# Kernel tuning notes

Hardware: AMD Instinct MI355X
Metric: run time of the kernel (lower is better)

## Reference

```python
import jax, jax.numpy as jnp
import numpy as np

B, C, T = 128, 9, 2048
R = T // 4            # reduced_timesteps after two MaxPool1d(2)
N = B * R             # total graph nodes
E_SINGLE = 8192       # edges per sample graph (avg degree 16 over R nodes)
HID = 128
OUT = 12


def setup_inputs():
    key = jax.random.key(0)
    ks = jax.random.split(key, 14)
    x = jax.random.normal(ks[0], (B, C, T), jnp.float32)
    # per-sample graph, replicated with offset i*R per batch element (as in forward)
    single = jax.random.randint(ks[1], (2, E_SINGLE), 0, R)
    offsets = (jnp.arange(B) * R)[None, :, None]
    edge_index = (single[:, None, :] + offsets).reshape(2, -1)  # [2, B*E_SINGLE]

    def lin(k, fan_in, shape):
        return jax.random.normal(k, shape, jnp.float32) / np.sqrt(fan_in)

    return {
        "x": x,
        "edge_index": edge_index,
        "conv1_w": lin(ks[2], C * 5, (16, C, 5)),
        "conv1_b": jnp.zeros((16,), jnp.float32),
        "conv2_w": lin(ks[3], 16 * 5, (32, 16, 5)),
        "conv2_b": jnp.zeros((32,), jnp.float32),
        "gcn1_w": lin(ks[4], 32, (32, HID)),
        "gcn1_b": jnp.zeros((HID,), jnp.float32),
        "gcn2_w": lin(ks[5], HID, (HID, HID)),
        "gcn2_b": jnp.zeros((HID,), jnp.float32),
        "fc_w": lin(ks[6], HID, (HID, OUT)),
        "fc_b": jnp.zeros((OUT,), jnp.float32),
    }


def _gcn_conv(h, edge_index, w, b, n):
    # PyG GCNConv: linear -> add self-loops -> sym-normalized sum aggregation -> + bias
    h = h @ w
    loops = jnp.arange(n)
    row = jnp.concatenate([edge_index[0], loops])  # source
    col = jnp.concatenate([edge_index[1], loops])  # target (aggregation)
    deg = jax.ops.segment_sum(jnp.ones(col.shape, h.dtype), col, num_segments=n)
    dis = jnp.where(deg > 0, jax.lax.rsqrt(jnp.maximum(deg, 1e-12)), 0.0)
    norm = dis[row] * dis[col]                      # [E+N]
    out = jax.ops.segment_sum(norm[:, None] * h[row], col, num_segments=n)
    return out + b


def _temporal_conv(x, w1, b1, w2, b2):
    dn = ("NCH", "OIH", "NCH")
    h = jax.lax.conv_general_dilated(x, w1, (1,), [(2, 2)], dimension_numbers=dn)
    h = jax.nn.relu(h + b1[None, :, None])
    h = jax.lax.reduce_window(h, -jnp.inf, jax.lax.max, (1, 1, 2), (1, 1, 2), "VALID")
    h = jax.lax.conv_general_dilated(h, w2, (1,), [(2, 2)], dimension_numbers=dn)
    h = jax.nn.relu(h + b2[None, :, None])
    h = jax.lax.reduce_window(h, -jnp.inf, jax.lax.max, (1, 1, 2), (1, 1, 2), "VALID")
    return h  # [B, 32, R]


def reference(x, edge_index, conv1_w, conv1_b, conv2_w, conv2_b,
              gcn1_w, gcn1_b, gcn2_w, gcn2_b, fc_w, fc_b):
    h = _temporal_conv(x, conv1_w, conv1_b, conv2_w, conv2_b)   # [B, 32, R]
    nodes = h.transpose(0, 2, 1).reshape(B * R, 32)             # [N, 32]
    g = jax.nn.relu(_gcn_conv(nodes, edge_index, gcn1_w, gcn1_b, N))
    g = jax.nn.relu(_gcn_conv(g, edge_index, gcn2_w, gcn2_b, N))
    g = g.reshape(B, R, HID).mean(axis=1)                       # [B, HID]
    return g @ fc_w + fc_b                                      # [B, OUT]
```

## Files before the change

kernel.cpp:

```cpp
#include <hip/hip_runtime.h>
#include <hip/hip_bf16.h>

#define BB   128
#define CIN  9
#define TT   2048
#define RR   512
#define NN   (BB*RR)
#define HID  128
#define NOUT 12

__global__ __launch_bounds__(256) void k_convs(const float* __restrict__ x,
        const float* __restrict__ w1, const float* __restrict__ b1,
        const float* __restrict__ w2, const float* __restrict__ b2,
        float* __restrict__ nodes, int* __restrict__ cnt,
        float* __restrict__ meanbuf) {
    __shared__ float sx[CIN][524];
    __shared__ float s1[16][260];
    __shared__ float sw1[16 * CIN * 5];
    __shared__ float sb1[16];
    __shared__ float sw2[32 * 16 * 5];
    __shared__ float sb2[32];
    int b  = blockIdx.x >> 2;
    int r0 = (blockIdx.x & 3) * 128;
    int tid = threadIdx.x;

    if (blockIdx.x == 0) { cnt[tid] = 0; cnt[tid + 256] = 0; }
    if (blockIdx.x < 64) meanbuf[blockIdx.x * 256 + tid] = 0.f;

    for (int idx = tid; idx < CIN * 524; idx += 256) {
        int c = idx / 524, j = idx - c * 524;
        int g = 4 * r0 - 6 + j;
        float v = 0.f;
        if (g >= 0 && g < TT) v = x[(b * CIN + c) * TT + g];
        sx[c][j] = v;
    }
    for (int idx = tid; idx < 16 * CIN * 5; idx += 256) sw1[idx] = w1[idx];
    for (int idx = tid; idx < 32 * 16 * 5; idx += 256) sw2[idx] = w2[idx];
    if (tid < 16) sb1[tid] = b1[tid];
    if (tid < 32) sb2[tid] = b2[tid];
    __syncthreads();

    for (int idx = tid; idx < 16 * 260; idx += 256) {
        int c1 = idx / 260, pp = idx - c1 * 260;
        int p = 2 * r0 - 2 + pp;
        float val = 0.f;
        if (p >= 0 && p < 1024) {
            float a0 = sb1[c1], a1 = a0;
#pragma unroll
            for (int c = 0; c < CIN; ++c) {
                float xv[6];
#pragma unroll
                for (int k = 0; k < 6; ++k) xv[k] = sx[c][2 * pp + k];
#pragma unroll
                for (int k = 0; k < 5; ++k) {
                    float wv = sw1[(c1 * CIN + c) * 5 + k];
                    a0 += xv[k]     * wv;
                    a1 += xv[k + 1] * wv;
                }
            }
            val = fmaxf(fmaxf(a0, a1), 0.f);
        }
        s1[c1][pp] = val;
    }
    __syncthreads();

    int rl   = tid & 127;
    int half = tid >> 7;
    float acc0[16], acc1[16];
#pragma unroll
    for (int o = 0; o < 16; ++o) { float bv = sb2[half * 16 + o]; acc0[o] = bv; acc1[o] = bv; }
#pragma unroll
    for (int c = 0; c < 16; ++c) {
        float xv[6];
#pragma unroll
        for (int k = 0; k < 6; ++k) xv[k] = s1[c][2 * rl + k];
#pragma unroll
        for (int o = 0; o < 16; ++o) {
            int oo = half * 16 + o;
#pragma unroll
            for (int k = 0; k < 5; ++k) {
                float wv = sw2[(oo * 16 + c) * 5 + k];
                acc0[o] += xv[k]     * wv;
                acc1[o] += xv[k + 1] * wv;
            }
        }
    }
    int n = b * RR + r0 + rl;
#pragma unroll
    for (int o = 0; o < 16; ++o) {
        int oo = half * 16 + o;
        nodes[n * 32 + oo] = fmaxf(fmaxf(acc0[o], acc1[o]), 0.f);
    }
}

__global__ __launch_bounds__(256) void k_deg512(const int* __restrict__ ei, int E,
        int es, int* __restrict__ cnt) {
    int i = blockIdx.x * 256 + threadIdx.x;
    if (i < es) atomicAdd(&cnt[ei[E + i]], 1);
}

__global__ __launch_bounds__(512) void k_scan512(const int* __restrict__ cnt, int es,
        int* __restrict__ rptr, int* __restrict__ cursor, float* __restrict__ dis) {
    __shared__ int sp[512];
    int t = threadIdx.x;
    int c = cnt[t];
    sp[t] = c;
    __syncthreads();
    for (int off = 1; off < 512; off <<= 1) {
        int v = sp[t];
        int add = (t >= off) ? sp[t - off] : 0;
        __syncthreads();
        sp[t] = v + add;
        __syncthreads();
    }
    int excl = sp[t] - c;
    rptr[t] = excl;
    cursor[t] = excl;
    if (t == 511) rptr[512] = es;
    dis[t] = rsqrtf((float)c + 1.0f);
}

__global__ __launch_bounds__(256) void k_scatter512(const int* __restrict__ ei, int E,
        int es, int* __restrict__ cursor, int* __restrict__ adj) {
    int i = blockIdx.x * 256 + threadIdx.x;
    if (i >= es) return;
    int row = ei[i];
    int col = ei[E + i];
    int pos = atomicAdd(&cursor[col], 1);
    adj[pos] = row;
}

__global__ __launch_bounds__(256) void k_gl1(const int* __restrict__ rptr,
        const int* __restrict__ adj, const float* __restrict__ dis,
        const float* __restrict__ nodes, const float* __restrict__ w,
        const float* __restrict__ bias, float* __restrict__ h) {
    __shared__ float srow[32][32];
    __shared__ float sw[32 * 128];
    int bid = (blockIdx.x & 7) * 256 + (blockIdx.x >> 3);
    int tid = threadIdx.x;
    int nbase = bid * 32;
    int b = nbase >> 9;
    const float* hb = nodes + (size_t)b * RR * 32;

    {
        const float4* src = (const float4*)w;
        float4* dst = (float4*)sw;
#pragma unroll
        for (int i = 0; i < 4; ++i) dst[tid + i * 256] = src[tid + i * 256];
    }

    int ln   = tid >> 3;
    int lane = tid & 7;
    int r = (nbase & 511) + ln;
    int s = rptr[r], e = rptr[r + 1];
    float dn = dis[r];
    float4 acc = make_float4(0.f, 0.f, 0.f, 0.f);
    for (int base = s; base < e; base += 8) {
        int j = base + lane;
        int src = 0; float nd = 0.f;
        if (j < e) { src = adj[j]; nd = dis[src]; }
        int cnt = min(8, e - base);
        int k = 0;
        for (; k + 4 <= cnt; k += 4) {
            int   s0 = __shfl(src, k, 8),     s1 = __shfl(src, k + 1, 8);
            int   s2 = __shfl(src, k + 2, 8), s3 = __shfl(src, k + 3, 8);
            float n0 = __shfl(nd, k, 8),      n1 = __shfl(nd, k + 1, 8);
            float n2 = __shfl(nd, k + 2, 8),  n3 = __shfl(nd, k + 3, 8);
            float4 v0 = *(const float4*)&hb[(size_t)s0 * 32 + lane * 4];
            float4 v1 = *(const float4*)&hb[(size_t)s1 * 32 + lane * 4];
            float4 v2 = *(const float4*)&hb[(size_t)s2 * 32 + lane * 4];
            float4 v3 = *(const float4*)&hb[(size_t)s3 * 32 + lane * 4];
            float w0 = dn * n0, w1 = dn * n1, w2 = dn * n2, w3 = dn * n3;
            acc.x += w0*v0.x + w1*v1.x + w2*v2.x + w3*v3.x;
            acc.y += w0*v0.y + w1*v1.y + w2*v2.y + w3*v3.y;
            acc.z += w0*v0.z + w1*v1.z + w2*v2.z + w3*v3.z;
            acc.w += w0*v0.w + w1*v1.w + w2*v2.w + w3*v3.w;
        }
        for (; k < cnt; ++k) {
            int   sk = __shfl(src, k, 8);
            float nk = __shfl(nd, k, 8);
            float4 v = *(const float4*)&hb[(size_t)sk * 32 + lane * 4];
            float wgt = dn * nk;
            acc.x += wgt * v.x; acc.y += wgt * v.y;
            acc.z += wgt * v.z; acc.w += wgt * v.w;
        }
    }
    {
        float4 v = *(const float4*)&hb[(size_t)r * 32 + lane * 4];
        float wgt = dn * dn;
        acc.x += wgt * v.x; acc.y += wgt * v.y;
        acc.z += wgt * v.z; acc.w += wgt * v.w;
    }
    *(float4*)&srow[ln][lane * 4] = acc;
    __syncthreads();

    int fq = tid & 31;
    int ng = tid >> 5;
    float a[4][4];
#pragma unroll
    for (int j = 0; j < 4; ++j)
#pragma unroll
        for (int q = 0; q < 4; ++q) a[j][q] = 0.f;
#pragma unroll
    for (int c = 0; c < 32; ++c) {
        float4 wv = *(const float4*)&sw[c * 128 + fq * 4];
#pragma unroll
        for (int j = 0; j < 4; ++j) {
            float xc = srow[ng * 4 + j][c];
            a[j][0] += xc * wv.x; a[j][1] += xc * wv.y;
            a[j][2] += xc * wv.z; a[j][3] += xc * wv.w;
        }
    }
    float4 bv = *(const float4*)&bias[fq * 4];
#pragma unroll
    for (int j = 0; j < 4; ++j) {
        float4 rr = make_float4(fmaxf(a[j][0] + bv.x, 0.f),
                                fmaxf(a[j][1] + bv.y, 0.f),
                                fmaxf(a[j][2] + bv.z, 0.f),
                                fmaxf(a[j][3] + bv.w, 0.f));
        *(float4*)&h[(size_t)(nbase + ng * 4 + j) * 128 + fq * 4] = rr;
    }
}

__global__ __launch_bounds__(256) void k_lin2(const float* __restrict__ g,
        const float* __restrict__ w, float* __restrict__ h) {
    __shared__ float srow[32 * 128];
    __shared__ float swc[64 * 128];
    int tid = threadIdx.x;
    int nbase = blockIdx.x * 32;
    {
        const float4* src = (const float4*)(g + (size_t)nbase * 128);
        float4* dst = (float4*)srow;
#pragma unroll
        for (int i = 0; i < 4; ++i) dst[tid + i * 256] = src[tid + i * 256];
    }
    int fq = tid & 31;
    int ng = tid >> 5;
    float acc[4][4];
#pragma unroll
    for (int j = 0; j < 4; ++j)
#pragma unroll
        for (int q = 0; q < 4; ++q) acc[j][q] = 0.f;

    for (int ch = 0; ch < 2; ++ch) {
        if (ch) __syncthreads();
        {
            const float4* src = (const float4*)(w + ch * 64 * 128);
            float4* dst = (float4*)swc;
#pragma unroll
            for (int i = 0; i < 8; ++i) dst[tid + i * 256] = src[tid + i * 256];
        }
        __syncthreads();
        int c0 = ch * 64;
#pragma unroll
        for (int c = 0; c < 64; ++c) {
            float4 wv = *(const float4*)&swc[c * 128 + fq * 4];
#pragma unroll
            for (int j = 0; j < 4; ++j) {
                float xc = srow[(ng * 4 + j) * 128 + c0 + c];
                acc[j][0] += xc * wv.x; acc[j][1] += xc * wv.y;
                acc[j][2] += xc * wv.z; acc[j][3] += xc * wv.w;
            }
        }
    }
#pragma unroll
    for (int j = 0; j < 4; ++j) {
        float4 r = make_float4(acc[j][0], acc[j][1], acc[j][2], acc[j][3]);
        *(float4*)&h[(size_t)(nbase + ng * 4 + j) * 128 + fq * 4] = r;
    }
}

__global__ __launch_bounds__(256) void k_gather128(const int* __restrict__ rptr,
        const int* __restrict__ adj, const float* __restrict__ dis,
        const float* __restrict__ h, const float* __restrict__ bias,
        float* __restrict__ meanbuf) {
    __shared__ float sred[8][128];
    int bid  = (blockIdx.x & 7) * 1024 + (blockIdx.x >> 3);
    int tid  = threadIdx.x;
    int g    = tid >> 5;
    int lane = tid & 31;
    int node = bid * 8 + g;
    int b = node >> 9;
    int r = node & 511;
    const float* hb = h + (size_t)b * RR * 128;
    int s = rptr[r], e = rptr[r + 1];
    float dn = dis[r];
    float4 acc = make_float4(0.f, 0.f, 0.f, 0.f);
    for (int base = s; base < e; base += 32) {
        int j = base + lane;
        int src = 0; float nd = 0.f;
        if (j < e) { src = adj[j]; nd = dis[src]; }
        int cnt = min(32, e - base);
        int k = 0;
        for (; k + 4 <= cnt; k += 4) {
            int   s0 = __shfl(src, k, 32),     s1 = __shfl(src, k + 1, 32);
            int   s2 = __shfl(src, k + 2, 32), s3 = __shfl(src, k + 3, 32);
            float n0 = __shfl(nd, k, 32),      n1 = __shfl(nd, k + 1, 32);
            float n2 = __shfl(nd, k + 2, 32),  n3 = __shfl(nd, k + 3, 32);
            float4 v0 = *(const float4*)&hb[(size_t)s0 * 128 + lane * 4];
            float4 v1 = *(const float4*)&hb[(size_t)s1 * 128 + lane * 4];
            float4 v2 = *(const float4*)&hb[(size_t)s2 * 128 + lane * 4];
            float4 v3 = *(const float4*)&hb[(size_t)s3 * 128 + lane * 4];
            float w0 = dn * n0, w1 = dn * n1, w2 = dn * n2, w3 = dn * n3;
            acc.x += w0*v0.x + w1*v1.x + w2*v2.x + w3*v3.x;
            acc.y += w0*v0.y + w1*v1.y + w2*v2.y + w3*v3.y;
            acc.z += w0*v0.z + w1*v1.z + w2*v2.z + w3*v3.z;
            acc.w += w0*v0.w + w1*v1.w + w2*v2.w + w3*v3.w;
        }
        for (; k < cnt; ++k) {
            int   sk = __shfl(src, k, 32);
            float nk = __shfl(nd, k, 32);
            float4 v = *(const float4*)&hb[(size_t)sk * 128 + lane * 4];
            float wgt = dn * nk;
            acc.x += wgt * v.x; acc.y += wgt * v.y;
            acc.z += wgt * v.z; acc.w += wgt * v.w;
        }
    }
    float4 v = *(const float4*)&hb[(size_t)r * 128 + lane * 4];
    float wgt = dn * dn;
    float4 bv = *(const float4*)&bias[lane * 4];
    acc.x = fmaxf(acc.x + wgt * v.x + bv.x, 0.f);
    acc.y = fmaxf(acc.y + wgt * v.y + bv.y, 0.f);
    acc.z = fmaxf(acc.z + wgt * v.z + bv.z, 0.f);
    acc.w = fmaxf(acc.w + wgt * v.w + bv.w, 0.f);
    *(float4*)&sred[g][lane * 4] = acc;
    __syncthreads();
    if (tid < 128) {
        float ssum = 0.f;
#pragma unroll
        for (int j = 0; j < 8; ++j) ssum += sred[j][tid];
        int sample = bid >> 6;
        unsafeAtomicAdd(&meanbuf[sample * 128 + tid], ssum * (1.0f / RR));
    }
}

__global__ __launch_bounds__(128) void k_fc(const float* __restrict__ meanbuf,
        const float* __restrict__ fw, const float* __restrict__ fb,
        float* __restrict__ out) {
    __shared__ float sm[HID];
    int b = blockIdx.x, f = threadIdx.x;
    sm[f] = meanbuf[b * HID + f];
    __syncthreads();
    if (f < NOUT) {
        float s = fb[f];
#pragma unroll
        for (int c = 0; c < HID; ++c) s += sm[c] * fw[c * NOUT + f];
        out[b * NOUT + f] = s;
    }
}

extern "C" void kernel_launch(void* const* d_in, const int* in_sizes, int n_in,
                              void* d_out, int out_size, void* d_ws, size_t ws_size,
                              hipStream_t stream) {
    const float* x   = (const float*)d_in[0];
    const int*   ei  = (const int*)d_in[1];
    const float* c1w = (const float*)d_in[2];
    const float* c1b = (const float*)d_in[3];
    const float* c2w = (const float*)d_in[4];
    const float* c2b = (const float*)d_in[5];
    const float* g1w = (const float*)d_in[6];
    const float* g1b = (const float*)d_in[7];
    const float* g2w = (const float*)d_in[8];
    const float* g2b = (const float*)d_in[9];
    const float* fw  = (const float*)d_in[10];
    const float* fb  = (const float*)d_in[11];
    float* out = (float*)d_out;
    int E  = in_sizes[1] / 2;
    int es = E / BB;

    char* ws = (char*)d_ws;
    float* nodes   = (float*)(ws);
    float* bufA    = (float*)(ws + (8u  << 20));
    float* bufC    = (float*)(ws + (40u << 20));
    int*   cnt     = (int*)  (ws + (72u << 20));
    int*   rptr    = (int*)  (ws + (72u << 20) + 4096);
    int*   cursor  = (int*)  (ws + (72u << 20) + 8192);
    float* dis     = (float*)(ws + (72u << 20) + 12288);
    int*   adj     = (int*)  (ws + (72u << 20) + 16384);
    float* meanbuf = (float*)(ws + (73u << 20));

    k_convs<<<BB * 4, 256, 0, stream>>>(x, c1w, c1b, c2w, c2b, nodes, cnt, meanbuf);

    k_deg512<<<(es + 255) / 256, 256, 0, stream>>>(ei, E, es, cnt);
    k_scan512<<<1, 512, 0, stream>>>(cnt, es, rptr, cursor, dis);
    k_scatter512<<<(es + 255) / 256, 256, 0, stream>>>(ei, E, es, cursor, adj);

    k_gl1<<<NN / 32, 256, 0, stream>>>(rptr, adj, dis, nodes, g1w, g1b, bufA);

    k_lin2<<<NN / 32, 256, 0, stream>>>(bufA, g2w, bufC);
    k_gather128<<<NN / 8, 256, 0, stream>>>(rptr, adj, dis, bufC, g2b, meanbuf);

    k_fc<<<BB, 128, 0, stream>>>(meanbuf, fw, fb, out);
}
```

Baseline: 212.4 us.

## Store GCN hidden activations in bf16, use MFMA for layer-2 linear, fuse CSR build

Hidden activations between the GCN layers are now stored as bf16, which halves the memory traffic of the layer-2 linear step and the neighbour gather. The second linear layer moves from scalar FP32 FMAs to bf16 MFMA 16x16x32 instructions, with the weight transposed into shared memory. The three CSR-build kernels (degree count, scan, scatter) are merged into a single one-block kernel that uses shared-memory atomics. Costs: reduced precision in the intermediates, each block re-converting the weights, and a serialised single-block graph build.

```diff
diff --git a/kernel.cpp b/kernel.cpp
--- a/kernel.cpp
+++ b/kernel.cpp
@@ -9,11 +9,22 @@
 #define HID  128
 #define NOUT 12
 
+typedef __attribute__((ext_vector_type(8))) short short8;
+typedef __attribute__((ext_vector_type(4))) float f32x4;
+
+static __device__ inline unsigned short f2bf(float f) {
+    unsigned int u = __float_as_uint(f);
+    unsigned int r = (u + 0x7fffu + ((u >> 16) & 1u)) >> 16;
+    return (unsigned short)r;
+}
+static __device__ inline float bf2f(unsigned short u) {
+    return __uint_as_float(((unsigned int)u) << 16);
+}
+
 __global__ __launch_bounds__(256) void k_convs(const float* __restrict__ x,
         const float* __restrict__ w1, const float* __restrict__ b1,
         const float* __restrict__ w2, const float* __restrict__ b2,
-        float* __restrict__ nodes, int* __restrict__ cnt,
-        float* __restrict__ meanbuf) {
+        float* __restrict__ nodes, float* __restrict__ meanbuf) {
     __shared__ float sx[CIN][524];
     __shared__ float s1[16][260];
     __shared__ float sw1[16 * CIN * 5];
@@ -24,7 +35,6 @@
     int r0 = (blockIdx.x & 3) * 128;
     int tid = threadIdx.x;
 
-    if (blockIdx.x == 0) { cnt[tid] = 0; cnt[tid + 256] = 0; }
     if (blockIdx.x < 64) meanbuf[blockIdx.x * 256 + tid] = 0.f;
 
     for (int idx = tid; idx < CIN * 524; idx += 256) {
@@ -93,17 +103,18 @@
     }
 }
 
-__global__ __launch_bounds__(256) void k_deg512(const int* __restrict__ ei, int E,
-        int es, int* __restrict__ cnt) {
-    int i = blockIdx.x * 256 + threadIdx.x;
-    if (i < es) atomicAdd(&cnt[ei[E + i]], 1);
-}
-
-__global__ __launch_bounds__(512) void k_scan512(const int* __restrict__ cnt, int es,
-        int* __restrict__ rptr, int* __restrict__ cursor, float* __restrict__ dis) {
+__global__ __launch_bounds__(512) void k_graph(const int* __restrict__ ei, int E,
+        int es, int* __restrict__ rptr, float* __restrict__ dis,
+        int* __restrict__ adj) {
+    __shared__ int lcnt[512];
     __shared__ int sp[512];
+    __shared__ int lcur[512];
     int t = threadIdx.x;
-    int c = cnt[t];
+    lcnt[t] = 0;
+    __syncthreads();
+    for (int i = t; i < es; i += 512) atomicAdd(&lcnt[ei[E + i]], 1);
+    __syncthreads();
+    int c = lcnt[t];
     sp[t] = c;
     __syncthreads();
     for (int off = 1; off < 512; off <<= 1) {
@@ -115,25 +126,21 @@
     }
     int excl = sp[t] - c;
     rptr[t] = excl;
-    cursor[t] = excl;
     if (t == 511) rptr[512] = es;
     dis[t] = rsqrtf((float)c + 1.0f);
-}
-
-__global__ __launch_bounds__(256) void k_scatter512(const int* __restrict__ ei, int E,
-        int es, int* __restrict__ cursor, int* __restrict__ adj) {
-    int i = blockIdx.x * 256 + threadIdx.x;
-    if (i >= es) return;
-    int row = ei[i];
-    int col = ei[E + i];
-    int pos = atomicAdd(&cursor[col], 1);
-    adj[pos] = row;
+    lcur[t] = excl;
+    __syncthreads();
+    for (int i = t; i < es; i += 512) {
+        int row = ei[i], col = ei[E + i];
+        int pos = atomicAdd(&lcur[col], 1);
+        adj[pos] = row;
+    }
 }
 
 __global__ __launch_bounds__(256) void k_gl1(const int* __restrict__ rptr,
         const int* __restrict__ adj, const float* __restrict__ dis,
         const float* __restrict__ nodes, const float* __restrict__ w,
-        const float* __restrict__ bias, float* __restrict__ h) {
+        const float* __restrict__ bias, unsigned short* __restrict__ h16) {
     __shared__ float srow[32][32];
     __shared__ float sw[32 * 128];
     int bid = (blockIdx.x & 7) * 256 + (blockIdx.x >> 3);
@@ -214,65 +221,73 @@
     float4 bv = *(const float4*)&bias[fq * 4];
 #pragma unroll
     for (int j = 0; j < 4; ++j) {
-        float4 rr = make_float4(fmaxf(a[j][0] + bv.x, 0.f),
-                                fmaxf(a[j][1] + bv.y, 0.f),
-                                fmaxf(a[j][2] + bv.z, 0.f),
-                                fmaxf(a[j][3] + bv.w, 0.f));
-        *(float4*)&h[(size_t)(nbase + ng * 4 + j) * 128 + fq * 4] = rr;
-    }
-}
-
-__global__ __launch_bounds__(256) void k_lin2(const float* __restrict__ g,
-        const float* __restrict__ w, float* __restrict__ h) {
-    __shared__ float srow[32 * 128];
-    __shared__ float swc[64 * 128];
+        ushort4 o;
+        o.x = f2bf(fmaxf(a[j][0] + bv.x, 0.f));
+        o.y = f2bf(fmaxf(a[j][1] + bv.y, 0.f));
+        o.z = f2bf(fmaxf(a[j][2] + bv.z, 0.f));
+        o.w = f2bf(fmaxf(a[j][3] + bv.w, 0.f));
+        *(ushort4*)&h16[(size_t)(nbase + ng * 4 + j) * 128 + fq * 4] = o;
+    }
+}
+
+__global__ __launch_bounds__(256) void k_lin2(const unsigned short* __restrict__ g16,
+        const float* __restrict__ w, unsigned short* __restrict__ h16) {
+    __shared__ unsigned short srow[64][136];
+    __shared__ unsigned short swT[128][136];
     int tid = threadIdx.x;
-    int nbase = blockIdx.x * 32;
+    int nbase = blockIdx.x * 64;
+
     {
-        const float4* src = (const float4*)(g + (size_t)nbase * 128);
-        float4* dst = (float4*)srow;
-#pragma unroll
-        for (int i = 0; i < 4; ++i) dst[tid + i * 256] = src[tid + i * 256];
-    }
-    int fq = tid & 31;
-    int ng = tid >> 5;
-    float acc[4][4];
-#pragma unroll
-    for (int j = 0; j < 4; ++j)
-#pragma unroll
-        for (int q = 0; q < 4; ++q) acc[j][q] = 0.f;
-
-    for (int ch = 0; ch < 2; ++ch) {
-        if (ch) __syncthreads();
-        {
-            const float4* src = (const float4*)(w + ch * 64 * 128);
-            float4* dst = (float4*)swc;
-#pragma unroll
-            for (int i = 0; i < 8; ++i) dst[tid + i * 256] = src[tid + i * 256];
-        }
-        __syncthreads();
-        int c0 = ch * 64;
-#pragma unroll
-        for (int c = 0; c < 64; ++c) {
-            float4 wv = *(const float4*)&swc[c * 128 + fq * 4];
-#pragma unroll
-            for (int j = 0; j < 4; ++j) {
-                float xc = srow[(ng * 4 + j) * 128 + c0 + c];
-                acc[j][0] += xc * wv.x; acc[j][1] += xc * wv.y;
-                acc[j][2] += xc * wv.z; acc[j][3] += xc * wv.w;
-            }
-        }
-    }
-#pragma unroll
-    for (int j = 0; j < 4; ++j) {
-        float4 r = make_float4(acc[j][0], acc[j][1], acc[j][2], acc[j][3]);
-        *(float4*)&h[(size_t)(nbase + ng * 4 + j) * 128 + fq * 4] = r;
+        const ushort4* src = (const ushort4*)(g16 + (size_t)nbase * 128);
+#pragma unroll
+        for (int i = 0; i < 8; ++i) {
+            int idx = tid + i * 256;
+            int row = idx >> 5, col4 = idx & 31;
+            ushort4 v = src[idx];
+            *(ushort4*)&srow[row][col4 * 4] = v;
+        }
+    }
+    {
+        for (int i = 0; i < 64; ++i) {
+            int idx = i * 256 + tid;
+            int c = idx >> 7, f = idx & 127;
+            swT[f][c] = f2bf(w[idx]);
+        }
+    }
+    __syncthreads();
+
+    int wv  = tid >> 6;
+    int lane = tid & 63;
+    int m0 = wv * 16;
+    int l15 = lane & 15;
+    int quad = lane >> 4;
+    f32x4 acc[8];
+#pragma unroll
+    for (int nt = 0; nt < 8; ++nt) acc[nt] = (f32x4){0.f, 0.f, 0.f, 0.f};
+#pragma unroll
+    for (int kc = 0; kc < 4; ++kc) {
+        int k0 = kc * 32 + quad * 8;
+        short8 a = *(const short8*)&srow[m0 + l15][k0];
+#pragma unroll
+        for (int nt = 0; nt < 8; ++nt) {
+            short8 b = *(const short8*)&swT[nt * 16 + l15][k0];
+            acc[nt] = __builtin_amdgcn_mfma_f32_16x16x32_bf16(a, b, acc[nt], 0, 0, 0);
+        }
+    }
+#pragma unroll
+    for (int nt = 0; nt < 8; ++nt) {
+#pragma unroll
+        for (int r = 0; r < 4; ++r) {
+            int row = m0 + quad * 4 + r;
+            int col = nt * 16 + l15;
+            h16[(size_t)(nbase + row) * 128 + col] = f2bf(acc[nt][r]);
+        }
     }
 }
 
 __global__ __launch_bounds__(256) void k_gather128(const int* __restrict__ rptr,
         const int* __restrict__ adj, const float* __restrict__ dis,
-        const float* __restrict__ h, const float* __restrict__ bias,
+        const unsigned short* __restrict__ h, const float* __restrict__ bias,
         float* __restrict__ meanbuf) {
     __shared__ float sred[8][128];
     int bid  = (blockIdx.x & 7) * 1024 + (blockIdx.x >> 3);
@@ -282,7 +297,7 @@
     int node = bid * 8 + g;
     int b = node >> 9;
     int r = node & 511;
-    const float* hb = h + (size_t)b * RR * 128;
+    const unsigned short* hb = h + (size_t)b * RR * 128;
     int s = rptr[r], e = rptr[r + 1];
     float dn = dis[r];
     float4 acc = make_float4(0.f, 0.f, 0.f, 0.f);
@@ -297,32 +312,32 @@
             int   s2 = __shfl(src, k + 2, 32), s3 = __shfl(src, k + 3, 32);
             float n0 = __shfl(nd, k, 32),      n1 = __shfl(nd, k + 1, 32);
             float n2 = __shfl(nd, k + 2, 32),  n3 = __shfl(nd, k + 3, 32);
-            float4 v0 = *(const float4*)&hb[(size_t)s0 * 128 + lane * 4];
-            float4 v1 = *(const float4*)&hb[(size_t)s1 * 128 + lane * 4];
-            float4 v2 = *(const float4*)&hb[(size_t)s2 * 128 + lane * 4];
-            float4 v3 = *(const float4*)&hb[(size_t)s3 * 128 + lane * 4];
+            ushort4 u0 = *(const ushort4*)&hb[(size_t)s0 * 128 + lane * 4];
+            ushort4 u1 = *(const ushort4*)&hb[(size_t)s1 * 128 + lane * 4];
+            ushort4 u2 = *(const ushort4*)&hb[(size_t)s2 * 128 + lane * 4];
+            ushort4 u3 = *(const ushort4*)&hb[(size_t)s3 * 128 + lane * 4];
             float w0 = dn * n0, w1 = dn * n1, w2 = dn * n2, w3 = dn * n3;
-            acc.x += w0*v0.x + w1*v1.x + w2*v2.x + w3*v3.x;
-            acc.y += w0*v0.y + w1*v1.y + w2*v2.y + w3*v3.y;
-            acc.z += w0*v0.z + w1*v1.z + w2*v2.z + w3*v3.z;
-            acc.w += w0*v0.w + w1*v1.w + w2*v2.w + w3*v3.w;
+            acc.x += w0*bf2f(u0.x) + w1*bf2f(u1.x) + w2*bf2f(u2.x) + w3*bf2f(u3.x);
+            acc.y += w0*bf2f(u0.y) + w1*bf2f(u1.y) + w2*bf2f(u2.y) + w3*bf2f(u3.y);
+            acc.z += w0*bf2f(u0.z) + w1*bf2f(u1.z) + w2*bf2f(u2.z) + w3*bf2f(u3.z);
+            acc.w += w0*bf2f(u0.w) + w1*bf2f(u1.w) + w2*bf2f(u2.w) + w3*bf2f(u3.w);
         }
         for (; k < cnt; ++k) {
             int   sk = __shfl(src, k, 32);
             float nk = __shfl(nd, k, 32);
-            float4 v = *(const float4*)&hb[(size_t)sk * 128 + lane * 4];
+            ushort4 u = *(const ushort4*)&hb[(size_t)sk * 128 + lane * 4];
             float wgt = dn * nk;
-            acc.x += wgt * v.x; acc.y += wgt * v.y;
-            acc.z += wgt * v.z; acc.w += wgt * v.w;
-        }
-    }
-    float4 v = *(const float4*)&hb[(size_t)r * 128 + lane * 4];
+            acc.x += wgt * bf2f(u.x); acc.y += wgt * bf2f(u.y);
+            acc.z += wgt * bf2f(u.z); acc.w += wgt * bf2f(u.w);
+        }
+    }
+    ushort4 u = *(const ushort4*)&hb[(size_t)r * 128 + lane * 4];
     float wgt = dn * dn;
     float4 bv = *(const float4*)&bias[lane * 4];
-    acc.x = fmaxf(acc.x + wgt * v.x + bv.x, 0.f);
-    acc.y = fmaxf(acc.y + wgt * v.y + bv.y, 0.f);
-    acc.z = fmaxf(acc.z + wgt * v.z + bv.z, 0.f);
-    acc.w = fmaxf(acc.w + wgt * v.w + bv.w, 0.f);
+    acc.x = fmaxf(acc.x + wgt * bf2f(u.x) + bv.x, 0.f);
+    acc.y = fmaxf(acc.y + wgt * bf2f(u.y) + bv.y, 0.f);
+    acc.z = fmaxf(acc.z + wgt * bf2f(u.z) + bv.z, 0.f);
+    acc.w = fmaxf(acc.w + wgt * bf2f(u.w) + bv.w, 0.f);
     *(float4*)&sred[g][lane * 4] = acc;
     __syncthreads();
     if (tid < 128) {
@@ -369,26 +384,22 @@
     int es = E / BB;
 
     char* ws = (char*)d_ws;
-    float* nodes   = (float*)(ws);
-    float* bufA    = (float*)(ws + (8u  << 20));
-    float* bufC    = (float*)(ws + (40u << 20));
-    int*   cnt     = (int*)  (ws + (72u << 20));
-    int*   rptr    = (int*)  (ws + (72u << 20) + 4096);
-    int*   cursor  = (int*)  (ws + (72u << 20) + 8192);
-    float* dis     = (float*)(ws + (72u << 20) + 12288);
-    int*   adj     = (int*)  (ws + (72u << 20) + 16384);
-    float* meanbuf = (float*)(ws + (73u << 20));
-
-    k_convs<<<BB * 4, 256, 0, stream>>>(x, c1w, c1b, c2w, c2b, nodes, cnt, meanbuf);
-
-    k_deg512<<<(es + 255) / 256, 256, 0, stream>>>(ei, E, es, cnt);
-    k_scan512<<<1, 512, 0, stream>>>(cnt, es, rptr, cursor, dis);
-    k_scatter512<<<(es + 255) / 256, 256, 0, stream>>>(ei, E, es, cursor, adj);
-
-    k_gl1<<<NN / 32, 256, 0, stream>>>(rptr, adj, dis, nodes, g1w, g1b, bufA);
-
-    k_lin2<<<NN / 32, 256, 0, stream>>>(bufA, g2w, bufC);
-    k_gather128<<<NN / 8, 256, 0, stream>>>(rptr, adj, dis, bufC, g2b, meanbuf);
+    float*          nodes   = (float*)(ws);
+    unsigned short* bufA16  = (unsigned short*)(ws + (8u  << 20));
+    unsigned short* bufC16  = (unsigned short*)(ws + (24u << 20));
+    int*   rptr    = (int*)  (ws + (40u << 20));
+    float* dis     = (float*)(ws + (40u << 20) + 4096);
+    int*   adj     = (int*)  (ws + (40u << 20) + 8192);
+    float* meanbuf = (float*)(ws + (41u << 20));
+
+    k_convs<<<BB * 4, 256, 0, stream>>>(x, c1w, c1b, c2w, c2b, nodes, meanbuf);
+
+    k_graph<<<1, 512, 0, stream>>>(ei, E, es, rptr, dis, adj);
+
+    k_gl1<<<NN / 32, 256, 0, stream>>>(rptr, adj, dis, nodes, g1w, g1b, bufA16);
+
+    k_lin2<<<NN / 64, 256, 0, stream>>>(bufA16, g2w, bufC16);
+    k_gather128<<<NN / 8, 256, 0, stream>>>(rptr, adj, dis, bufC16, g2b, meanbuf);
 
     k_fc<<<BB, 128, 0, stream>>>(meanbuf, fw, fb, out);
 }
```

Result: faster. 200.7 us (-5.5%).
